# Optimization experiments

Hardware: AMD Instinct MI355X
Metric: run time of the kernel (lower is better)

The kernel has to match this reference:

```python
import jax, jax.numpy as jnp
import numpy as np
import math

INNER = 96
EPS = 1e-8  # torch CosineSimilarity eps


def _proj(x, W1, W2):
    # nn.Linear(C,C,bias=False) -> ReLU -> nn.Linear(C,inner,bias=False)
    return jax.nn.relu(x @ W1) @ W2


def _cos(a, b):
    # torch CosineSimilarity(dim=-1): dot / (max(||a||,eps)*max(||b||,eps))
    num = jnp.sum(a * b, axis=-1)
    na = jnp.maximum(jnp.linalg.norm(a, axis=-1), EPS)
    nb = jnp.maximum(jnp.linalg.norm(b, axis=-1), EPS)
    return num / (na * nb)


def setup_inputs() -> dict:
    key = jax.random.key(0)
    ks = jax.random.split(key, 8)
    B, C, H, W = 128, 768, 7, 7
    sc1 = 1.0 / math.sqrt(C)
    inp = {
        "features_a": jax.random.normal(ks[0], (B, C, H, W), jnp.float32),
        "features_b": jax.random.normal(ks[1], (B, C, H, W), jnp.float32),
        "Wq1": jax.random.normal(ks[2], (C, C), jnp.float32) * sc1,
        "Wq2": jax.random.normal(ks[3], (C, INNER), jnp.float32) * sc1,
        "Wk1": jax.random.normal(ks[4], (C, C), jnp.float32) * sc1,
        "Wk2": jax.random.normal(ks[5], (C, INNER), jnp.float32) * sc1,
        "Wv1": jax.random.normal(ks[6], (C, C), jnp.float32) * sc1,
        "Wv2": jax.random.normal(ks[7], (C, INNER), jnp.float32) * sc1,
    }
    return inp


def reference(features_a, features_b, Wq1, Wq2, Wk1, Wk2, Wv1, Wv2):
    B, C = features_a.shape[0], features_a.shape[1]
    # [B, C, H, W] -> [B, S, C]
    fa = features_a.reshape(B, C, -1).transpose(0, 2, 1)
    fb = features_b.reshape(features_b.shape[0], C, -1).transpose(0, 2, 1)

    qa, ka, va = _proj(fa, Wq1, Wq2), _proj(fa, Wk1, Wk2), _proj(fa, Wv1, Wv2)
    qb, kb, vb = _proj(fb, Wq1, Wq2), _proj(fb, Wk1, Wk2), _proj(fb, Wv1, Wv2)

    scale = 1.0 / math.sqrt(INNER)

    # query_b vs key_a: [Bb, Ba, Sq, Sk]
    scores_ba = jnp.einsum('bqe,ake->baqk', qb, ka) * scale
    probs_ba = jax.nn.softmax(scores_ba, axis=-1)
    aligned_a = jnp.einsum('baqk,ake->baqe', probs_ba, va)  # [Bb, Ba, S, inner]

    # query_a vs key_b: [Bb, Ba, Sq, Sk]
    scores_ab = jnp.einsum('aqe,bke->baqk', qa, kb) * scale
    probs_ab = jax.nn.softmax(scores_ab, axis=-1)
    aligned_b = jnp.einsum('baqk,bke->baqe', probs_ab, vb)  # [Bb, Ba, S, inner]

    sim = _cos(va[None, :, :, :], aligned_b) + _cos(vb[:, None, :, :], aligned_a)
    return sim.mean(-1)  # [Bb, Ba]
```

## Files before the change

kernel.cpp:

```cpp
#include <hip/hip_runtime.h>
#include <hip/hip_bf16.h>
#include <math.h>

typedef __attribute__((ext_vector_type(8))) short bf16x8;
typedef __attribute__((ext_vector_type(4))) float f32x4;

#define MROWS 12544
#define CDIM 768
#define INNER 96
#define S49 49
#define NSIDE 6272
#define SCALE 0.10206207261596577f
#define SCALE_EXP2 ((float)(0.10206207261596577 * 1.4426950408889634))

__device__ __forceinline__ unsigned short f2bf(float f) {
  union { float f; unsigned u; } v; v.f = f;
  unsigned u = v.u;
  return (unsigned short)((u + 0x7fffu + ((u >> 16) & 1u)) >> 16);
}
__device__ __forceinline__ float bf2f(unsigned short h) {
  union { unsigned u; float f; } v; v.u = ((unsigned)h) << 16;
  return v.f;
}
__device__ __forceinline__ unsigned pack_bf16_rn(float a, float b) {
  union { float f; unsigned u; } ua, ub; ua.f = a; ub.f = b;
  return __builtin_amdgcn_perm(ub.u + 0x8000u, ua.u + 0x8000u, 0x07060302u);
}

__device__ __forceinline__ void gld16(const unsigned short* g, unsigned short* l) {
  __builtin_amdgcn_global_load_lds(
      (const __attribute__((address_space(1))) unsigned int*)(g),
      (__attribute__((address_space(3))) unsigned int*)(l), 16, 0, 0);
}

__global__ __launch_bounds__(256) void prep_all(
    const float* __restrict__ fa, const float* __restrict__ fb,
    const float* __restrict__ w10, const float* __restrict__ w11,
    const float* __restrict__ w12, const float* __restrict__ w20,
    const float* __restrict__ w21, const float* __restrict__ w22,
    unsigned short* __restrict__ X,
    unsigned short* __restrict__ W1T, unsigned short* __restrict__ W2T,
    unsigned short* __restrict__ VtKpad) {
  const int t = threadIdx.x;
  int id = blockIdx.x;
  if (id < 3072) {
    __shared__ float T[64][50];
    const int z = id / 1536; id -= z * 1536;
    const int ct = id % 12, img = id / 12;
    const float* feat = z ? fb : fa;
    const float* src = feat + (size_t)img * (CDIM * S49) + (size_t)ct * 64 * S49;
    for (int idx = t; idx < 64 * S49; idx += 256) {
      int cc = idx / S49, s = idx - cc * S49;
      T[cc][s] = src[cc * S49 + s];
    }
    __syncthreads();
    unsigned short* dst = X + (size_t)(z * 128 + img) * S49 * CDIM + ct * 64;
    for (int idx = t; idx < S49 * 64; idx += 256) {
      int s = idx >> 6, cc = idx & 63;
      dst[(size_t)s * CDIM + cc] = f2bf(T[cc][s]);
    }
  } else if (id < 5016) {
    __shared__ float T[32][33];
    id -= 3072;
    const float* src;
    unsigned short* dst;
    int C, ctile, rtile;
    if (id < 1728) {
      int wdx = id / 576, tid = id - wdx * 576;
      ctile = tid % 24; rtile = tid / 24;
      src = wdx == 0 ? w10 : (wdx == 1 ? w11 : w12);
      dst = W1T + (size_t)wdx * CDIM * CDIM;
      C = CDIM;
    } else {
      id -= 1728;
      int wdx = id / 72, tid = id - wdx * 72;
      ctile = tid % 3; rtile = tid / 3;
      src = wdx == 0 ? w20 : (wdx == 1 ? w21 : w22);
      dst = W2T + (size_t)wdx * INNER * CDIM;
      C = INNER;
    }
    const int c0 = ctile * 32, r0 = rtile * 32;
    for (int idx = t; idx < 1024; idx += 256) {
      int rr = idx >> 5, cc = idx & 31;
      T[rr][cc] = src[(size_t)(r0 + rr) * C + c0 + cc];
    }
    __syncthreads();
    for (int idx = t; idx < 1024; idx += 256) {
      int rr = idx >> 5, cc = idx & 31;
      dst[(size_t)(c0 + rr) * CDIM + r0 + cc] = f2bf(T[cc][rr]);
    }
  } else {
    id -= 5016;
    ushort4* p4 = (ushort4*)VtKpad;
    const ushort4 z = make_ushort4(0, 0, 0, 0);
#pragma unroll
    for (int i = 0; i < 32; i++)
      p4[(size_t)id * 8192 + i * 256 + t] = z;
  }
}

__global__ __launch_bounds__(256) void gemm1b3(const unsigned short* __restrict__ X,
                                               const unsigned short* __restrict__ W1T,
                                               unsigned short* __restrict__ H,
                                               int wbase, int hsel) {
  __shared__ __align__(16) unsigned short As[128 * 64];
  __shared__ __align__(16) unsigned short Bs[128 * 64];
  const int t = threadIdx.x;
  const int lane = t & 63, w = t >> 6;
  const int lr = lane & 15, lq = lane >> 4;
  const int wm = w & 1, wn = w >> 1;
  const int m0 = blockIdx.y * 128, n0 = blockIdx.x * 128;
  const int wdx = blockIdx.z + wbase;
  const unsigned short* W1w = W1T + (size_t)wdx * CDIM * CDIM;
  unsigned short* Hw = H + (hsel ? (size_t)wdx * MROWS * CDIM : 0);
  const f32x4 z4 = {0.f, 0.f, 0.f, 0.f};
  f32x4 acc[4][4] = {{z4, z4, z4, z4}, {z4, z4, z4, z4},
                     {z4, z4, z4, z4}, {z4, z4, z4, z4}};

  for (int k0 = 0; k0 < CDIM; k0 += 64) {
    __syncthreads();
#pragma unroll
    for (int j = 0; j < 4; j++) {
      int idx = t + j * 256;
      int row = idx >> 3, col = (idx & 7) * 8;
      gld16(X + (size_t)(m0 + row) * CDIM + k0 + col, As + idx * 8);
      gld16(W1w + (size_t)(n0 + row) * CDIM + k0 + col, Bs + idx * 8);
    }
    __syncthreads();
#pragma unroll
    for (int ks = 0; ks < 2; ks++) {
      bf16x8 a[4], b[4];
#pragma unroll
      for (int mt = 0; mt < 4; mt++)
        a[mt] = *(const bf16x8*)(As + (wm * 64 + mt * 16 + lr) * 64 + ks * 32 + lq * 8);
#pragma unroll
      for (int nt = 0; nt < 4; nt++)
        b[nt] = *(const bf16x8*)(Bs + (wn * 64 + nt * 16 + lr) * 64 + ks * 32 + lq * 8);
#pragma unroll
      for (int mt = 0; mt < 4; mt++)
#pragma unroll
        for (int nt = 0; nt < 4; nt++)
          acc[mt][nt] = __builtin_amdgcn_mfma_f32_16x16x32_bf16(a[mt], b[nt], acc[mt][nt], 0, 0, 0);
    }
  }
#pragma unroll
  for (int mt = 0; mt < 4; mt++)
#pragma unroll
    for (int nt = 0; nt < 4; nt++)
#pragma unroll
      for (int r = 0; r < 4; r++) {
        int m = m0 + wm * 64 + mt * 16 + lq * 4 + r;
        int n = n0 + wn * 64 + nt * 16 + lr;
        Hw[(size_t)m * CDIM + n] = f2bf(fmaxf(acc[mt][nt][r], 0.f));
      }
}

#define LDK 72
__global__ __launch_bounds__(256) void gemm2b3(const unsigned short* __restrict__ H,
                                               const unsigned short* __restrict__ W2T,
                                               unsigned short* __restrict__ QKV,
                                               unsigned short* __restrict__ Kpad,
                                               unsigned short* __restrict__ Vt,
                                               float* __restrict__ vnorm,
                                               int wbase, int hsel) {
  __shared__ __align__(16) unsigned short As[64 * LDK];
  __shared__ __align__(16) unsigned short Bs[96 * LDK];
  const int t = threadIdx.x;
  const int lane = t & 63, w = t >> 6;
  const int lr = lane & 15, lq = lane >> 4;
  const int m0 = blockIdx.x * 64;
  const int wdx = blockIdx.y + wbase;
  const unsigned short* Hw = H + (hsel ? (size_t)wdx * MROWS * CDIM : 0);
  const unsigned short* W2w = W2T + (size_t)wdx * INNER * CDIM;
  const f32x4 z4 = {0.f, 0.f, 0.f, 0.f};
  f32x4 acc[6] = {z4, z4, z4, z4, z4, z4};

  for (int k0 = 0; k0 < CDIM; k0 += 64) {
    __syncthreads();
    for (int c = t; c < 512; c += 256) {
      int r = c >> 3, kc = (c & 7) * 8;
      *(uint4*)(As + r * LDK + kc) = *(const uint4*)(Hw + (size_t)(m0 + r) * CDIM + k0 + kc);
    }
    for (int c = t; c < 768; c += 256) {
      int r = c >> 3, kc = (c & 7) * 8;
      *(uint4*)(Bs + r * LDK + kc) = *(const uint4*)(W2w + (size_t)r * CDIM + k0 + kc);
    }
    __syncthreads();
#pragma unroll
    for (int kk = 0; kk < 2; kk++) {
      bf16x8 a = *(const bf16x8*)(As + (w * 16 + lr) * LDK + kk * 32 + lq * 8);
#pragma unroll
      for (int nt = 0; nt < 6; nt++) {
        bf16x8 b = *(const bf16x8*)(Bs + (nt * 16 + lr) * LDK + kk * 32 + lq * 8);
        acc[nt] = __builtin_amdgcn_mfma_f32_16x16x32_bf16(a, b, acc[nt], 0, 0, 0);
      }
    }
  }
  float nsq[4] = {0.f, 0.f, 0.f, 0.f};
#pragma unroll
  for (int nt = 0; nt < 6; nt++)
#pragma unroll
    for (int r = 0; r < 4; r++) {
      int m = m0 + w * 16 + lq * 4 + r;
      int e = nt * 16 + lr;
      float v = acc[nt][r];
      int img = m / 49, s = m - img * 49;
      if (wdx == 0) {
        QKV[(size_t)m * INNER + e] = f2bf(v * SCALE_EXP2);
      } else if (wdx == 1) {
        Kpad[(size_t)(img * 64 + s) * INNER + e] = f2bf(v);
      } else {
        QKV[(size_t)(2 * MROWS + m) * INNER + e] = f2bf(v);
        Vt[(size_t)img * (INNER * 64) + e * 64 + s] = f2bf(v);
        nsq[r] += v * v;
      }
    }
  if (wdx == 2) {
#pragma unroll
    for (int r = 0; r < 4; r++) {
      float p = nsq[r];
      p += __shfl_xor(p, 1, 16);
      p += __shfl_xor(p, 2, 16);
      p += __shfl_xor(p, 4, 16);
      p += __shfl_xor(p, 8, 16);
      if (lr == 0) vnorm[m0 + w * 16 + lq * 4 + r] = sqrtf(p);
    }
  }
}

#define LQS 104
#define LVS 72
__global__ __launch_bounds__(256) void attn7(const unsigned short* __restrict__ Qp,
                                             const unsigned short* __restrict__ Kpad,
                                             const unsigned short* __restrict__ V,
                                             const unsigned short* __restrict__ Vt,
                                             const float* __restrict__ vnorm,
                                             float* __restrict__ cosbuf) {
  __shared__ __align__(16) unsigned short Ks[64 * LQS];
  __shared__ __align__(16) unsigned short Vts[96 * LVS];
  __shared__ __align__(16) unsigned short Ps[4][32 * LVS];

  const int t = threadIdx.x;
  const int lane = t & 63, w = t >> 6;
  const int lr = lane & 15, lq = lane >> 4;
  const f32x4 z4 = {0.f, 0.f, 0.f, 0.f};

  int bx = blockIdx.x;
  const int dir = bx / 392; bx -= dir * 392;
  const int chunk = bx >> 3, fg = bx & 7;
  const int r0 = chunk * 128;
  const int qbase = dir * NSIDE;

  const int rk0 = t / 12, ck0 = (t - rk0 * 12) * 8;
  const int rv0 = t >> 3, cv0 = (t & 7) * 8;

  bf16x8 qf[2][3];
#pragma unroll
  for (int qt = 0; qt < 2; qt++) {
    const int qrow = qbase + r0 + w * 32 + qt * 16 + lr;
#pragma unroll
    for (int ks = 0; ks < 3; ks++)
      qf[qt][ks] = *(const bf16x8*)(Qp + (size_t)qrow * INNER + ks * 32 + lq * 8);
  }
  float rv[2][6][4], invvn[2];
#pragma unroll
  for (int qt = 0; qt < 2; qt++) {
    const int qrow = qbase + r0 + w * 32 + qt * 16 + lr;
    invvn[qt] = 1.f / fmaxf(vnorm[qrow], 1e-8f);
#pragma unroll
    for (int et = 0; et < 6; et++) {
      ushort4 u = *(const ushort4*)(V + (size_t)qrow * INNER + et * 16 + lq * 4);
      rv[qt][et][0] = bf2f(u.x); rv[qt][et][1] = bf2f(u.y);
      rv[qt][et][2] = bf2f(u.z); rv[qt][et][3] = bf2f(u.w);
    }
  }

  unsigned short* Pw = &Ps[w][0];
  const int kimg0 = (dir == 0 ? 128 : 0) + fg * 16;
  for (int fi = 0; fi < 16; fi++) {
    const int f = fg * 16 + fi;
    const unsigned short* kg = Kpad + (size_t)(kimg0 + fi) * (64 * INNER);
    const unsigned short* vg = Vt + (size_t)(kimg0 + fi) * (INNER * 64);
    __syncthreads();
#pragma unroll
    for (int i = 0; i < 3; i++) {
      int rk = rk0 + i * 21, ck = ck0 + ((i * 4) % 12) * 8;
      (void)rk; (void)ck;
    }
    {
      int i0 = t, i1 = t + 256, i2 = t + 512;
      int r_0 = i0 / 12, c_0 = (i0 - r_0 * 12) * 8;
      int r_1 = i1 / 12, c_1 = (i1 - r_1 * 12) * 8;
      int r_2 = i2 / 12, c_2 = (i2 - r_2 * 12) * 8;
      *(uint4*)(Ks + r_0 * LQS + c_0) = *(const uint4*)(kg + r_0 * INNER + c_0);
      *(uint4*)(Ks + r_1 * LQS + c_1) = *(const uint4*)(kg + r_1 * INNER + c_1);
      *(uint4*)(Ks + r_2 * LQS + c_2) = *(const uint4*)(kg + r_2 * INNER + c_2);
      int v1 = rv0 + 32, v2 = rv0 + 64;
      *(uint4*)(Vts + rv0 * LVS + cv0) = *(const uint4*)(vg + rv0 * 64 + cv0);
      *(uint4*)(Vts + v1 * LVS + cv0) = *(const uint4*)(vg + v1 * 64 + cv0);
      *(uint4*)(Vts + v2 * LVS + cv0) = *(const uint4*)(vg + v2 * 64 + cv0);
    }
    __syncthreads();
    f32x4 s4[2][4] = {{z4, z4, z4, z4}, {z4, z4, z4, z4}};
#pragma unroll
    for (int ks = 0; ks < 3; ks++) {
#pragma unroll
      for (int kt = 0; kt < 4; kt++) {
        bf16x8 a = *(const bf16x8*)(Ks + (kt * 16 + lr) * LQS + ks * 32 + lq * 8);
        s4[0][kt] = __builtin_amdgcn_mfma_f32_16x16x32_bf16(a, qf[0][ks], s4[0][kt], 0, 0, 0);
        s4[1][kt] = __builtin_amdgcn_mfma_f32_16x16x32_bf16(a, qf[1][ks], s4[1][kt], 0, 0, 0);
      }
    }
#pragma unroll
    for (int qt = 0; qt < 2; qt++)
#pragma unroll
      for (int kt = 0; kt < 4; kt++) {
        float e0 = __builtin_exp2f(s4[qt][kt][0]);
        float e1 = __builtin_exp2f(s4[qt][kt][1]);
        float e2 = __builtin_exp2f(s4[qt][kt][2]);
        float e3 = __builtin_exp2f(s4[qt][kt][3]);
        uint2 pk = make_uint2(pack_bf16_rn(e0, e1), pack_bf16_rn(e2, e3));
        *(uint2*)(Pw + (qt * 16 + lr) * LVS + kt * 16 + lq * 4) = pk;
      }
    f32x4 pv[2][6] = {{z4, z4, z4, z4, z4, z4}, {z4, z4, z4, z4, z4, z4}};
#pragma unroll
    for (int ks = 0; ks < 2; ks++) {
      bf16x8 b0 = *(const bf16x8*)(Pw + (0 * 16 + lr) * LVS + ks * 32 + lq * 8);
      bf16x8 b1 = *(const bf16x8*)(Pw + (1 * 16 + lr) * LVS + ks * 32 + lq * 8);
#pragma unroll
      for (int et = 0; et < 6; et++) {
        bf16x8 a = *(const bf16x8*)(Vts + (et * 16 + lr) * LVS + ks * 32 + lq * 8);
        pv[0][et] = __builtin_amdgcn_mfma_f32_16x16x32_bf16(a, b0, pv[0][et], 0, 0, 0);
        pv[1][et] = __builtin_amdgcn_mfma_f32_16x16x32_bf16(a, b1, pv[1][et], 0, 0, 0);
      }
    }
#pragma unroll
    for (int qt = 0; qt < 2; qt++) {
      float d = 0.f, nn = 0.f;
#pragma unroll
      for (int et = 0; et < 6; et++)
#pragma unroll
        for (int r = 0; r < 4; r++) {
          float al = pv[qt][et][r];
          d += al * rv[qt][et][r];
          nn += al * al;
        }
      d += __shfl_xor(d, 16, 64);  d += __shfl_xor(d, 32, 64);
      nn += __shfl_xor(nn, 16, 64); nn += __shfl_xor(nn, 32, 64);
      if (lane < 16) {
        float cv = d * __frsqrt_rn(fmaxf(nn, 1e-40f)) * invvn[qt];
        cosbuf[(size_t)(dir * 128 + f) * NSIDE + r0 + w * 32 + qt * 16 + lr] = cv;
      }
    }
  }
}

__global__ __launch_bounds__(256) void reduce_out(const float* __restrict__ cosbuf,
                                                  float* __restrict__ out) {
  const int t = threadIdx.x, lane = t & 63, wv = t >> 6;
  const int pair = blockIdx.x * 4 + wv;
  const int bb = pair >> 7, aa = pair & 127;
  float v = 0.f;
  if (lane < S49) {
    v  = cosbuf[(size_t)bb * NSIDE + aa * S49 + lane];
    v += cosbuf[(size_t)(128 + aa) * NSIDE + bb * S49 + lane];
  }
  for (int m = 1; m < 64; m <<= 1) v += __shfl_xor(v, m, 64);
  if (lane == 0) out[pair] = v * (1.f / 49.f);
}

extern "C" void kernel_launch(void* const* d_in, const int* in_sizes, int n_in,
                              void* d_out, int out_size, void* d_ws, size_t ws_size,
                              hipStream_t stream) {
  const float* fa  = (const float*)d_in[0];
  const float* fb  = (const float*)d_in[1];
  const float* W1[3] = {(const float*)d_in[2], (const float*)d_in[4], (const float*)d_in[6]};
  const float* W2[3] = {(const float*)d_in[3], (const float*)d_in[5], (const float*)d_in[7]};
  float* out = (float*)d_out;

  unsigned short* p = (unsigned short*)d_ws;
  unsigned short* Xbf = p;                 p += (size_t)MROWS * CDIM;
  unsigned short* W1T = p;                 p += (size_t)3 * CDIM * CDIM;
  unsigned short* W2T = p;                 p += (size_t)3 * INNER * CDIM;
  unsigned short* QKV = p;                 p += (size_t)3 * MROWS * INNER;
  unsigned short* Vt  = p;                 p += (size_t)256 * INNER * 64;
  unsigned short* Kpad = p;                p += (size_t)256 * 64 * INNER;
  float* vnorm = (float*)p;                p += (size_t)MROWS * 2;
  float* cosbuf = (float*)p;               p += (size_t)256 * NSIDE * 2;
  unsigned short* H = p;                   p += (size_t)3 * MROWS * CDIM;
  const size_t need_batched = (size_t)(p - (unsigned short*)d_ws) * 2;
  const int batched = ws_size >= need_batched;

  prep_all<<<dim3(5112), 256, 0, stream>>>(fa, fb, W1[0], W1[1], W1[2],
                                           W2[0], W2[1], W2[2],
                                           Xbf, W1T, W2T, Vt );
  if (batched) {
    gemm1b3<<<dim3(CDIM / 128, MROWS / 128, 3), 256, 0, stream>>>(Xbf, W1T, H, 0, 1);
    gemm2b3<<<dim3(MROWS / 64, 3), 256, 0, stream>>>(H, W2T, QKV, Kpad, Vt, vnorm, 0, 1);
  } else {
    for (int wdx = 0; wdx < 3; wdx++) {
      gemm1b3<<<dim3(CDIM / 128, MROWS / 128, 1), 256, 0, stream>>>(Xbf, W1T, H, wdx, 0);
      gemm2b3<<<dim3(MROWS / 64, 1), 256, 0, stream>>>(H, W2T, QKV, Kpad, Vt, vnorm, wdx, 0);
    }
  }
  attn7<<<dim3(2 * 392), 256, 0, stream>>>(
      QKV, Kpad, QKV + (size_t)2 * MROWS * INNER, Vt, vnorm, cosbuf);
  reduce_out<<<dim3(4096), 256, 0, stream>>>(cosbuf, out);
}
```

Measured before the change: 309.4 us.

## Double-buffer K/V tiles in attention via direct global-to-LDS loads with XOR swizzle

The attention kernel now keeps two LDS buffers for the key and transposed-value tiles and prefetches the next image's tiles while computing on the current one. The loads use a gld16 helper, apparently a direct global-to-LDS copy. Padded row strides are replaced by a rotation swizzle of the 16-byte column chunks to avoid bank conflicts. This is meant to hide global load latency and drop one barrier per iteration. In exchange it doubles LDS use for K/V, which may lower occupancy, and it relies on the swizzle index math and the wait semantics of the async loads being correct.

```diff
diff --git a/kernel.cpp b/kernel.cpp
--- a/kernel.cpp
+++ b/kernel.cpp
@@ -228,16 +228,15 @@
   }
 }
 
-#define LQS 104
 #define LVS 72
-__global__ __launch_bounds__(256) void attn7(const unsigned short* __restrict__ Qp,
+__global__ __launch_bounds__(256) void attn8(const unsigned short* __restrict__ Qp,
                                              const unsigned short* __restrict__ Kpad,
                                              const unsigned short* __restrict__ V,
                                              const unsigned short* __restrict__ Vt,
                                              const float* __restrict__ vnorm,
                                              float* __restrict__ cosbuf) {
-  __shared__ __align__(16) unsigned short Ks[64 * LQS];
-  __shared__ __align__(16) unsigned short Vts[96 * LVS];
+  __shared__ __align__(16) unsigned short KsD[2][64 * INNER];
+  __shared__ __align__(16) unsigned short VtD[2][INNER * 64];
   __shared__ __align__(16) unsigned short Ps[4][32 * LVS];
 
   const int t = threadIdx.x;
@@ -251,8 +250,29 @@
   const int r0 = chunk * 128;
   const int qbase = dir * NSIDE;
 
-  const int rk0 = t / 12, ck0 = (t - rk0 * 12) * 8;
-  const int rv0 = t >> 3, cv0 = (t & 7) * 8;
+  int goK[3], goV[3], lo[3];
+#pragma unroll
+  for (int j = 0; j < 3; j++) {
+    int l = (w * 3 + j) * 64 + lane;
+    lo[j] = l * 8;
+    int rK = l / 12, scK = l - rK * 12;
+    int ccK = scK - ((rK >> 1) & 7); if (ccK < 0) ccK += 12;
+    goK[j] = rK * INNER + ccK * 8;
+    int rV = l >> 3, scV = l & 7;
+    int ccV = (scV - (rV & 7)) & 7;
+    goV[j] = rV * 64 + ccV * 8;
+  }
+  int rdK[3], rdV[2];
+#pragma unroll
+  for (int ks = 0; ks < 3; ks++) {
+    int sc = (ks * 4 + lq + ((lr >> 1) & 7)) % 12;
+    rdK[ks] = lr * INNER + sc * 8;
+  }
+#pragma unroll
+  for (int ks = 0; ks < 2; ks++) {
+    int sc = (ks * 4 + lq + (lr & 7)) & 7;
+    rdV[ks] = lr * 64 + sc * 8;
+  }
 
   bf16x8 qf[2][3];
 #pragma unroll
@@ -277,36 +297,37 @@
 
   unsigned short* Pw = &Ps[w][0];
   const int kimg0 = (dir == 0 ? 128 : 0) + fg * 16;
+  {
+    const unsigned short* kg = Kpad + (size_t)kimg0 * (64 * INNER);
+    const unsigned short* vg = Vt + (size_t)kimg0 * (INNER * 64);
+#pragma unroll
+    for (int j = 0; j < 3; j++) {
+      gld16(kg + goK[j], &KsD[0][0] + lo[j]);
+      gld16(vg + goV[j], &VtD[0][0] + lo[j]);
+    }
+  }
   for (int fi = 0; fi < 16; fi++) {
     const int f = fg * 16 + fi;
-    const unsigned short* kg = Kpad + (size_t)(kimg0 + fi) * (64 * INNER);
-    const unsigned short* vg = Vt + (size_t)(kimg0 + fi) * (INNER * 64);
-    __syncthreads();
-#pragma unroll
-    for (int i = 0; i < 3; i++) {
-      int rk = rk0 + i * 21, ck = ck0 + ((i * 4) % 12) * 8;
-      (void)rk; (void)ck;
-    }
-    {
-      int i0 = t, i1 = t + 256, i2 = t + 512;
-      int r_0 = i0 / 12, c_0 = (i0 - r_0 * 12) * 8;
-      int r_1 = i1 / 12, c_1 = (i1 - r_1 * 12) * 8;
-      int r_2 = i2 / 12, c_2 = (i2 - r_2 * 12) * 8;
-      *(uint4*)(Ks + r_0 * LQS + c_0) = *(const uint4*)(kg + r_0 * INNER + c_0);
-      *(uint4*)(Ks + r_1 * LQS + c_1) = *(const uint4*)(kg + r_1 * INNER + c_1);
-      *(uint4*)(Ks + r_2 * LQS + c_2) = *(const uint4*)(kg + r_2 * INNER + c_2);
-      int v1 = rv0 + 32, v2 = rv0 + 64;
-      *(uint4*)(Vts + rv0 * LVS + cv0) = *(const uint4*)(vg + rv0 * 64 + cv0);
-      *(uint4*)(Vts + v1 * LVS + cv0) = *(const uint4*)(vg + v1 * 64 + cv0);
-      *(uint4*)(Vts + v2 * LVS + cv0) = *(const uint4*)(vg + v2 * 64 + cv0);
-    }
-    __syncthreads();
+    __syncthreads();
+    if (fi < 15) {
+      const unsigned short* kg = Kpad + (size_t)(kimg0 + fi + 1) * (64 * INNER);
+      const unsigned short* vg = Vt + (size_t)(kimg0 + fi + 1) * (INNER * 64);
+      unsigned short* kd = &KsD[1 - (fi & 1)][0];
+      unsigned short* vd = &VtD[1 - (fi & 1)][0];
+#pragma unroll
+      for (int j = 0; j < 3; j++) {
+        gld16(kg + goK[j], kd + lo[j]);
+        gld16(vg + goV[j], vd + lo[j]);
+      }
+    }
+    const unsigned short* KsC = &KsD[fi & 1][0];
+    const unsigned short* VtC = &VtD[fi & 1][0];
     f32x4 s4[2][4] = {{z4, z4, z4, z4}, {z4, z4, z4, z4}};
 #pragma unroll
     for (int ks = 0; ks < 3; ks++) {
 #pragma unroll
       for (int kt = 0; kt < 4; kt++) {
-        bf16x8 a = *(const bf16x8*)(Ks + (kt * 16 + lr) * LQS + ks * 32 + lq * 8);
+        bf16x8 a = *(const bf16x8*)(KsC + kt * (16 * INNER) + rdK[ks]);
         s4[0][kt] = __builtin_amdgcn_mfma_f32_16x16x32_bf16(a, qf[0][ks], s4[0][kt], 0, 0, 0);
         s4[1][kt] = __builtin_amdgcn_mfma_f32_16x16x32_bf16(a, qf[1][ks], s4[1][kt], 0, 0, 0);
       }
@@ -329,7 +350,7 @@
       bf16x8 b1 = *(const bf16x8*)(Pw + (1 * 16 + lr) * LVS + ks * 32 + lq * 8);
 #pragma unroll
       for (int et = 0; et < 6; et++) {
-        bf16x8 a = *(const bf16x8*)(Vts + (et * 16 + lr) * LVS + ks * 32 + lq * 8);
+        bf16x8 a = *(const bf16x8*)(VtC + et * (16 * 64) + rdV[ks]);
         pv[0][et] = __builtin_amdgcn_mfma_f32_16x16x32_bf16(a, b0, pv[0][et], 0, 0, 0);
         pv[1][et] = __builtin_amdgcn_mfma_f32_16x16x32_bf16(a, b1, pv[1][et], 0, 0, 0);
       }
@@ -403,7 +424,7 @@
       gemm2b3<<<dim3(MROWS / 64, 1), 256, 0, stream>>>(H, W2T, QKV, Kpad, Vt, vnorm, wdx, 0);
     }
   }
-  attn7<<<dim3(2 * 392), 256, 0, stream>>>(
+  attn8<<<dim3(2 * 392), 256, 0, stream>>>(
       QKV, Kpad, QKV + (size_t)2 * MROWS * INNER, Vt, vnorm, cosbuf);
   reduce_out<<<dim3(4096), 256, 0, stream>>>(cosbuf, out);
 }
```

Result: no change. 306.3 us (-1.0%).
